# Optimization experiments

Hardware: AMD Instinct MI355X
Metric: run time of the kernel (lower is better)

The kernel has to match this reference:

```python
import jax, jax.numpy as jnp
import numpy as np

S_STRIDE = 4
NS = 4
SHIFT_RANGE = 2 * NS + 1  # 9 -> 81 shifts
MASK_THRESH = 10.0


def setup_inputs() -> dict:
    key = jax.random.key(0)
    k1, k2, k3, k4 = jax.random.split(key, 4)
    N, C, H, W = 2, 8, 1024, 1024
    ms_img = jax.random.uniform(k1, (N, C, H, W), dtype=jnp.float32)
    target = jax.random.uniform(k2, (N, C, H, W), dtype=jnp.float32)
    ms_img_o = jax.random.uniform(k3, (N, C, H, W), dtype=jnp.float32)
    fr_pan = jax.random.uniform(k4, (N, 1, H, W), dtype=jnp.float32)
    return {"ms_img": ms_img, "target": target, "ms_img_o": ms_img_o, "fr_pan": fr_pan}


def _min_shift_loss(ms_img, target):
    # Equivalent to torch: reflect-pad target, unfold 9x9 dilated-by-4 windows,
    # per-shift sum_C |ms - shifted_target|, then min over the 81 shifts.
    # Computed with a running min to avoid the (N,C,81,H,W) intermediate.
    N, C, H, W = target.shape
    p = NS * S_STRIDE
    tpad = jnp.pad(target, ((0, 0), (0, 0), (p, p), (p, p)), mode="reflect")
    min_sloss = None
    for i in range(SHIFT_RANGE):
        for j in range(SHIFT_RANGE):
            shifted = tpad[:, :, i * S_STRIDE:i * S_STRIDE + H, j * S_STRIDE:j * S_STRIDE + W]
            sl = jnp.sum(jnp.abs(ms_img - shifted), axis=1)  # (N, H, W)
            min_sloss = sl if min_sloss is None else jnp.minimum(min_sloss, sl)
    return min_sloss


def _normalize(x):
    # min-max normalize to [0,1] over the whole tensor (normalize_torch)
    lo = jnp.min(x)
    hi = jnp.max(x)
    return (x - lo) / (hi - lo)


def reference(ms_img, target, ms_img_o, fr_pan):
    min_sloss = _min_shift_loss(ms_img, target)           # (N, H, W)
    ms_o_gray = jnp.mean(ms_img_o, axis=1)                # (N, H, W)
    mask_gray = _normalize(jnp.abs(ms_o_gray - fr_pan[:, 0])) * 255.0
    mask = mask_gray > MASK_THRESH
    masked_sum = jnp.sum(jnp.where(mask, min_sloss, 0.0))
    cnt = jnp.sum(mask).astype(min_sloss.dtype)
    # mean over masked pixels; 0 if mask empty (matches torch early-return 0)
    return jnp.where(cnt > 0, masked_sum / jnp.maximum(cnt, 1.0), 0.0)
```

## Files before the change

kernel.cpp:

```cpp
#include <hip/hip_runtime.h>

#define WW 1024
#define HH 1024
#define NIMG 2
#define NCH 8
#define HWSZ (HH * WW)
#define CHW (NCH * HWSZ)
#define NBLK_MAIN 1024
#define WS_SUM 4096
#define WS_CNT 4097
#define WS_TKT 4098
#define WS_DV16 4352
#define WS_QT (4352 + HWSZ)
#define RECU4 320
#define SLOTU 1280

typedef unsigned int uint;

__device__ __forceinline__ uint pknorm(float a, float b) {
    uint d;
    asm("v_cvt_pknorm_u16_f32 %0, %1, %2" : "=v"(d) : "v"(a), "v"(b));
    return d;
}
__device__ __forceinline__ uint sadu8(uint a, uint b, uint c) {
    uint d;
    asm("v_sad_u8 %0, %1, %2, %3" : "=v"(d) : "v"(a), "v"(b), "v"(c));
    return d;
}
__device__ __forceinline__ uint q8(float x) {
    return (uint)__float2int_rn(x * 255.f);
}
__device__ __forceinline__ int reflect_idx(int t) {
    if (t < 0) t = -t;
    if (t > HH - 1) t = 2 * (HH - 1) - t;
    return t;
}
__device__ __forceinline__ int gp2slot(int gp) {
    return (gp & 1) ? (68 + (gp >> 1)) : (gp >> 1);
}

#define GLD16(g, l)                                                         \
    __builtin_amdgcn_global_load_lds(                                       \
        (const __attribute__((address_space(1))) uint*)(g),                 \
        (__attribute__((address_space(3))) uint*)(l), 16, 0, 0)

__global__ __launch_bounds__(256) void k_pre(const float* __restrict__ tgt,
                                             uint4* __restrict__ qt4,
                                             const float* __restrict__ msO,
                                             const float* __restrict__ pan,
                                             float* __restrict__ wsF,
                                             uint* __restrict__ dv16) {
    const int b3 = blockIdx.x;
    const int m3 = b3 % 3;
    const int t = threadIdx.x;

    if (m3 != 2) {
        int b = (b3 / 3) * 2 + m3;
        int row = b & 1023;
        int np = b >> 10;
        int n = np >> 1, p = np & 1;
        const float* c0 = tgt + (size_t)(n * NCH + 4 * p) * HWSZ + (size_t)row * WW;

        float4 v0 = *(const float4*)(c0 + 4 * t);
        float4 v1 = *(const float4*)(c0 + HWSZ + 4 * t);
        float4 v2 = *(const float4*)(c0 + 2 * HWSZ + 4 * t);
        float4 v3 = *(const float4*)(c0 + 3 * HWSZ + 4 * t);
        uint4 u;
        u.x = q8(v0.x) | (q8(v1.x) << 8) | (q8(v2.x) << 16) | (q8(v3.x) << 24);
        u.y = q8(v0.y) | (q8(v1.y) << 8) | (q8(v2.y) << 16) | (q8(v3.y) << 24);
        u.z = q8(v0.z) | (q8(v1.z) << 8) | (q8(v2.z) << 16) | (q8(v3.z) << 24);
        u.w = q8(v0.w) | (q8(v1.w) << 8) | (q8(v2.w) << 16) | (q8(v3.w) << 24);

        size_t rb = ((size_t)((n << 10) + row)) * 2;
        int h1 = t >> 7;
        int gp = (t & 127) + 4;
        qt4[(rb + h1) * RECU4 + p * 136 + gp2slot(gp)] = u;
        if (t >= 124 && t < 128)
            qt4[(rb + 1) * RECU4 + p * 136 + gp2slot(t - 124)] = u;
        if (t >= 128 && t < 132)
            qt4[(rb + 0) * RECU4 + p * 136 + gp2slot(t - 128 + 132)] = u;
        if (t < 32) {
            int which = t >> 4, m = t & 15;
            int pc = which ? (528 + m) : m;
            int j = which ? (1022 - m) : (16 - m);
            uint val = q8(c0[j]) | (q8(c0[j + HWSZ]) << 8) |
                       (q8(c0[j + 2 * HWSZ]) << 16) | (q8(c0[j + 3 * HWSZ]) << 24);
            uint* recU = (uint*)(qt4 + (rb + which) * RECU4);
            recU[p * 544 + gp2slot(pc >> 2) * 4 + (pc & 3)] = val;
        }
    } else {
        int b = b3 / 3;
        int gid = b * 256 + t;
        int base = gid * 4;
        int n = base >> 20;
        int hw = base & (HWSZ - 1);
        const float* po = msO + (size_t)n * CHW + hw;
        float sx = 0.f, sy = 0.f, sz = 0.f, sw = 0.f;
#pragma unroll
        for (int c = 0; c < NCH; ++c) {
            float4 v = *(const float4*)(po + c * HWSZ);
            sx += v.x; sy += v.y; sz += v.z; sw += v.w;
        }
        float4 pv = *(const float4*)(pan + (size_t)n * HWSZ + hw);
        float4 d;
        d.x = fabsf(sx * 0.125f - pv.x);
        d.y = fabsf(sy * 0.125f - pv.y);
        d.z = fabsf(sz * 0.125f - pv.z);
        d.w = fabsf(sw * 0.125f - pv.w);
        uint2 dpk;
        dpk.x = pknorm(d.x, d.y);
        dpk.y = pknorm(d.z, d.w);
        *(uint2*)(dv16 + (base >> 1)) = dpk;

        float m = fminf(fminf(d.x, d.y), fminf(d.z, d.w));
        float M = fmaxf(fmaxf(d.x, d.y), fmaxf(d.z, d.w));
#pragma unroll
        for (int off = 32; off > 0; off >>= 1) {
            m = fminf(m, __shfl_down(m, off));
            M = fmaxf(M, __shfl_down(M, off));
        }
        __shared__ float sm[4], sM[4];
        int wid = t >> 6, lane = t & 63;
        if (lane == 0) { sm[wid] = m; sM[wid] = M; }
        __syncthreads();
        if (t == 0) {
            wsF[b] = fminf(fminf(sm[0], sm[1]), fminf(sm[2], sm[3]));
            wsF[2048 + b] = fmaxf(fmaxf(sM[0], sM[1]), fmaxf(sM[2], sM[3]));
            if (b == 0) {
                wsF[WS_SUM] = 0.f;
                wsF[WS_CNT] = 0.f;
                ((unsigned*)wsF)[WS_TKT] = 0u;
            }
        }
    }
}

__global__ __launch_bounds__(64) void k_main(const float* __restrict__ ms,
                                             const uint4* __restrict__ qt4,
                                             float* __restrict__ wsF,
                                             const uint* __restrict__ dv16,
                                             float* __restrict__ out) {
    __shared__ __align__(16) uint ldsU[10 * SLOTU];
    const int t = threadIdx.x;
    const int b = blockIdx.x;
    const int xcd = b & 7;
    const int q = b >> 3;
    const int n = q >> 6;
    const int r = q & 63;
    const int hb = r >> 5;
    const int w = r & 31;
    const int h0 = xcd * 128 + 16 * (w >> 2) + (w & 3);
    const int w0 = hb * 512 + 8 * t;

    float lmin = 1.0e38f, lmax = -1.0e38f;
#pragma unroll
    for (int k = 0; k < 8; ++k) {
        float4 v = ((const float4*)wsF)[k * 64 + t];
        float4 x = ((const float4*)(wsF + 2048))[k * 64 + t];
        lmin = fminf(lmin, fminf(fminf(v.x, v.y), fminf(v.z, v.w)));
        lmax = fmaxf(lmax, fmaxf(fmaxf(x.x, x.y), fmaxf(x.z, x.w)));
    }

    const size_t recStride2 = 2;
    const size_t nBase = ((size_t)n << 10);
#pragma unroll 1
    for (int s = 0; s < 10; ++s) {
        int row = reflect_idx(h0 + 4 * (s - 4));
        const uint* rec = (const uint*)(qt4 + ((nBase + row) * recStride2 + hb) * RECU4);
#pragma unroll
        for (int c = 0; c < 5; ++c)
            GLD16(rec + c * 256 + 4 * t, &ldsU[s * SLOTU + c * 256]);
    }

#pragma unroll
    for (int off = 32; off > 0; off >>= 1) {
        lmin = fminf(lmin, __shfl_xor(lmin, off));
        lmax = fmaxf(lmax, __shfl_xor(lmax, off));
    }
    const float thresh = lmin + (lmax - lmin) * (10.0f / 255.0f);
    const float inv16 = 1.0f / 65535.0f;
    const float inv8 = 1.0f / 255.0f;

    asm volatile("s_waitcnt vmcnt(0)" ::: "memory");

    float lsum = 0.f, lcnt = 0.f;

#pragma unroll 1
    for (int k = 0; k < 4; ++k) {
        const int oh = h0 + 4 * k;

        const float* msBase = ms + (size_t)n * CHW + (size_t)oh * WW + w0;
        float4 A[2][4][2];
#pragma unroll
        for (int p = 0; p < 2; ++p)
#pragma unroll
            for (int cc = 0; cc < 4; ++cc) {
                A[p][cc][0] = *(const float4*)(msBase + (size_t)(4 * p + cc) * HWSZ);
                A[p][cc][1] = *(const float4*)(msBase + (size_t)(4 * p + cc) * HWSZ + 4);
            }
        uint4 dq = *(const uint4*)(dv16 + (((size_t)n * HWSZ + (size_t)oh * WW + w0) >> 1));

        if (k == 1 || k == 2) {
            int prow = reflect_idx(h0 + 4 * (k + 5));
            const uint* rec = (const uint*)(qt4 + ((nBase + prow) * recStride2 + hb) * RECU4);
#pragma unroll
            for (int c = 0; c < 5; ++c)
                GLD16(rec + c * 256 + 4 * t, &ldsU[(k - 1) * SLOTU + c * 256]);
        }

        uint msq[2][8];
#pragma unroll
        for (int p = 0; p < 2; ++p) {
#pragma unroll
            for (int half = 0; half < 2; ++half) {
                float4 c0 = A[p][0][half], c1 = A[p][1][half],
                       c2 = A[p][2][half], c3 = A[p][3][half];
                msq[p][4 * half + 0] = q8(c0.x) | (q8(c1.x) << 8) | (q8(c2.x) << 16) | (q8(c3.x) << 24);
                msq[p][4 * half + 1] = q8(c0.y) | (q8(c1.y) << 8) | (q8(c2.y) << 16) | (q8(c3.y) << 24);
                msq[p][4 * half + 2] = q8(c0.z) | (q8(c1.z) << 8) | (q8(c2.z) << 16) | (q8(c3.z) << 24);
                msq[p][4 * half + 3] = q8(c0.w) | (q8(c1.w) << 8) | (q8(c2.w) << 16) | (q8(c3.w) << 24);
            }
        }

        uint minv[8];
#pragma unroll
        for (int p = 0; p < 8; ++p) minv[p] = 0xffffffffu;

#pragma unroll 1
        for (int di = 0; di < 9; ++di) {
            int slot = k + di; if (slot >= 10) slot -= 10;
            const uint* sb = &ldsU[slot * SLOTU];
            uint4 winE[2][5], winO[2][5];
#pragma unroll
            for (int p = 0; p < 2; ++p)
#pragma unroll
                for (int qq = 0; qq < 5; ++qq) {
                    winE[p][qq] = *(const uint4*)(sb + p * 544 + 4 * (t + qq));
                    winO[p][qq] = *(const uint4*)(sb + p * 544 + 272 + 4 * (t + qq));
                }
            uint acc[8];
#pragma unroll
            for (int dj = 0; dj < 9; ++dj) {
#pragma unroll
                for (int p = 0; p < 8; ++p) acc[p] = 0;
#pragma unroll
                for (int p = 0; p < 2; ++p) {
                    uint4 lo = (dj & 1) ? winO[p][(dj - 1) >> 1] : winE[p][dj >> 1];
                    uint4 hi = (dj & 1) ? winE[p][(dj + 1) >> 1] : winO[p][dj >> 1];
                    acc[0] = sadu8(msq[p][0], lo.x, acc[0]);
                    acc[1] = sadu8(msq[p][1], lo.y, acc[1]);
                    acc[2] = sadu8(msq[p][2], lo.z, acc[2]);
                    acc[3] = sadu8(msq[p][3], lo.w, acc[3]);
                    acc[4] = sadu8(msq[p][4], hi.x, acc[4]);
                    acc[5] = sadu8(msq[p][5], hi.y, acc[5]);
                    acc[6] = sadu8(msq[p][6], hi.z, acc[6]);
                    acc[7] = sadu8(msq[p][7], hi.w, acc[7]);
                }
#pragma unroll
                for (int p = 0; p < 8; ++p) minv[p] = min(minv[p], acc[p]);
            }
        }
        asm volatile("s_waitcnt vmcnt(0)" ::: "memory");

        uint dw[4] = {dq.x, dq.y, dq.z, dq.w};
#pragma unroll
        for (int p = 0; p < 4; ++p) {
            float d0 = (float)(dw[p] & 0xffffu) * inv16;
            float d1 = (float)(dw[p] >> 16) * inv16;
            if (d0 > thresh) { lsum += (float)minv[2 * p] * inv8; lcnt += 1.f; }
            if (d1 > thresh) { lsum += (float)minv[2 * p + 1] * inv8; lcnt += 1.f; }
        }
    }

#pragma unroll
    for (int off = 32; off > 0; off >>= 1) {
        lsum += __shfl_down(lsum, off);
        lcnt += __shfl_down(lcnt, off);
    }
    if (t == 0) {
        atomicAdd(&wsF[WS_SUM], lsum);
        atomicAdd(&wsF[WS_CNT], lcnt);
        __threadfence();
        unsigned tk = atomicAdd((unsigned*)&wsF[WS_TKT], 1u);
        if (tk == NBLK_MAIN - 1) {
            float s = atomicAdd(&wsF[WS_SUM], 0.f);
            float c = atomicAdd(&wsF[WS_CNT], 0.f);
            out[0] = (c > 0.f) ? (s / fmaxf(c, 1.f)) : 0.f;
        }
    }
}

extern "C" void kernel_launch(void* const* d_in, const int* in_sizes, int n_in,
                              void* d_out, int out_size, void* d_ws, size_t ws_size,
                              hipStream_t stream) {
    const float* ms  = (const float*)d_in[0];
    const float* tgt = (const float*)d_in[1];
    const float* msO = (const float*)d_in[2];
    const float* pan = (const float*)d_in[3];
    float* out = (float*)d_out;
    float* wsF = (float*)d_ws;
    uint* dv16 = (uint*)d_ws + WS_DV16;
    uint4* qt4 = (uint4*)((uint*)d_ws + WS_QT);

    k_pre<<<6144, 256, 0, stream>>>(tgt, qt4, msO, pan, wsF, dv16);
    k_main<<<NBLK_MAIN, 64, 0, stream>>>(ms, qt4, wsF, dv16, out);
}
```

Before: 276.6 us.

## Split main kernel work across two waves sharing twelve LDS row slots

New measurement: 258.5 us. 6.5% less time.

```diff
diff --git a/kernel.cpp b/kernel.cpp
--- a/kernel.cpp
+++ b/kernel.cpp
@@ -13,7 +13,8 @@
 #define WS_DV16 4352
 #define WS_QT (4352 + HWSZ)
 #define RECU4 320
-#define SLOTU 1280
+#define SLOTC 1088
+#define NSLOT 12
 
 typedef unsigned int uint;
 
@@ -135,13 +136,15 @@
     }
 }
 
-__global__ __launch_bounds__(64) void k_main(const float* __restrict__ ms,
-                                             const uint4* __restrict__ qt4,
-                                             float* __restrict__ wsF,
-                                             const uint* __restrict__ dv16,
-                                             float* __restrict__ out) {
-    __shared__ __align__(16) uint ldsU[10 * SLOTU];
-    const int t = threadIdx.x;
+__global__ __launch_bounds__(128) void k_main(const float* __restrict__ ms,
+                                              const uint4* __restrict__ qt4,
+                                              float* __restrict__ wsF,
+                                              const uint* __restrict__ dv16,
+                                              float* __restrict__ out) {
+    __shared__ __align__(16) uint ldsU[NSLOT * SLOTC];
+    __shared__ float sS[2], sC[2];
+    const int t = threadIdx.x & 63;
+    const int wv = threadIdx.x >> 6;
     const int b = blockIdx.x;
     const int xcd = b & 7;
     const int q = b >> 3;
@@ -161,15 +164,17 @@
         lmax = fmaxf(lmax, fmaxf(fmaxf(x.x, x.y), fmaxf(x.z, x.w)));
     }
 
-    const size_t recStride2 = 2;
     const size_t nBase = ((size_t)n << 10);
 #pragma unroll 1
-    for (int s = 0; s < 10; ++s) {
+    for (int i = 0; i < 6; ++i) {
+        int s = 6 * wv + i;
         int row = reflect_idx(h0 + 4 * (s - 4));
-        const uint* rec = (const uint*)(qt4 + ((nBase + row) * recStride2 + hb) * RECU4);
-#pragma unroll
-        for (int c = 0; c < 5; ++c)
-            GLD16(rec + c * 256 + 4 * t, &ldsU[s * SLOTU + c * 256]);
+        const uint* rec = (const uint*)(qt4 + ((nBase + row) * 2 + hb) * RECU4);
+#pragma unroll
+        for (int c = 0; c < 4; ++c)
+            GLD16(rec + c * 256 + 4 * t, &ldsU[s * SLOTC + c * 256]);
+        if (t < 16)
+            GLD16(rec + 1024 + 4 * t, &ldsU[s * SLOTC + 1024]);
     }
 
 #pragma unroll
@@ -182,11 +187,13 @@
     const float inv8 = 1.0f / 255.0f;
 
     asm volatile("s_waitcnt vmcnt(0)" ::: "memory");
+    __syncthreads();
 
     float lsum = 0.f, lcnt = 0.f;
 
 #pragma unroll 1
-    for (int k = 0; k < 4; ++k) {
+    for (int ko = 0; ko < 2; ++ko) {
+        const int k = 2 * wv + ko;
         const int oh = h0 + 4 * k;
 
         const float* msBase = ms + (size_t)n * CHW + (size_t)oh * WW + w0;
@@ -199,14 +206,6 @@
                 A[p][cc][1] = *(const float4*)(msBase + (size_t)(4 * p + cc) * HWSZ + 4);
             }
         uint4 dq = *(const uint4*)(dv16 + (((size_t)n * HWSZ + (size_t)oh * WW + w0) >> 1));
-
-        if (k == 1 || k == 2) {
-            int prow = reflect_idx(h0 + 4 * (k + 5));
-            const uint* rec = (const uint*)(qt4 + ((nBase + prow) * recStride2 + hb) * RECU4);
-#pragma unroll
-            for (int c = 0; c < 5; ++c)
-                GLD16(rec + c * 256 + 4 * t, &ldsU[(k - 1) * SLOTU + c * 256]);
-        }
 
         uint msq[2][8];
 #pragma unroll
@@ -228,8 +227,7 @@
 
 #pragma unroll 1
         for (int di = 0; di < 9; ++di) {
-            int slot = k + di; if (slot >= 10) slot -= 10;
-            const uint* sb = &ldsU[slot * SLOTU];
+            const uint* sb = &ldsU[(k + di) * SLOTC];
             uint4 winE[2][5], winO[2][5];
 #pragma unroll
             for (int p = 0; p < 2; ++p)
@@ -260,7 +258,6 @@
                 for (int p = 0; p < 8; ++p) minv[p] = min(minv[p], acc[p]);
             }
         }
-        asm volatile("s_waitcnt vmcnt(0)" ::: "memory");
 
         uint dw[4] = {dq.x, dq.y, dq.z, dq.w};
 #pragma unroll
@@ -277,9 +274,11 @@
         lsum += __shfl_down(lsum, off);
         lcnt += __shfl_down(lcnt, off);
     }
-    if (t == 0) {
-        atomicAdd(&wsF[WS_SUM], lsum);
-        atomicAdd(&wsF[WS_CNT], lcnt);
+    if (t == 0) { sS[wv] = lsum; sC[wv] = lcnt; }
+    __syncthreads();
+    if (threadIdx.x == 0) {
+        atomicAdd(&wsF[WS_SUM], sS[0] + sS[1]);
+        atomicAdd(&wsF[WS_CNT], sC[0] + sC[1]);
         __threadfence();
         unsigned tk = atomicAdd((unsigned*)&wsF[WS_TKT], 1u);
         if (tk == NBLK_MAIN - 1) {
@@ -303,5 +302,5 @@
     uint4* qt4 = (uint4*)((uint*)d_ws + WS_QT);
 
     k_pre<<<6144, 256, 0, stream>>>(tgt, qt4, msO, pan, wsF, dv16);
-    k_main<<<NBLK_MAIN, 64, 0, stream>>>(ms, qt4, wsF, dv16, out);
-}
+    k_main<<<NBLK_MAIN, 128, 0, stream>>>(ms, qt4, wsF, dv16, out);
+}
```
